# Performance work log

Hardware: AMD Instinct MI355X
Metric: run time of the kernel (lower is better)

The kernel has to match this reference:

```python
import jax, jax.numpy as jnp
import numpy as np

B, S, D = 64, 8192, 128  # batch, source length, hidden (enc == dec)


def setup_inputs() -> dict:
    key = jax.random.key(0)
    ks = jax.random.split(key, 7)
    s = 1.0 / np.sqrt(D)
    return {
        "input": jax.random.normal(ks[0], (B, D), jnp.float32),
        "context": jax.random.normal(ks[1], (B, S, D), jnp.float32),
        "W_enc": jax.random.uniform(ks[2], (D, D), jnp.float32, -s, s),
        "b_enc": jax.random.uniform(ks[3], (D,), jnp.float32, -s, s),
        "W_dec": jax.random.uniform(ks[4], (D, D), jnp.float32, -s, s),
        "b_dec": jax.random.uniform(ks[5], (D,), jnp.float32, -s, s),
        "W_out": jax.random.uniform(ks[6], (D, 2 * D), jnp.float32, -s, s),  # no bias
    }


def reference(input, context, W_enc, b_enc, W_dec, b_dec, W_out):
    # projected_context = tanh(lin_encoder(context))  [B, S, D]
    pc = jnp.tanh(jnp.einsum("bse,de->bsd", context, W_enc) + b_enc)
    # q = tanh(lin_decoder(input))  [B, D]
    q = jnp.tanh(input @ W_dec.T + b_dec)
    # attention scores via bmm(projected_context, q): [B, S]
    scores = jnp.einsum("bsd,bd->bs", pc, q)
    attn = jax.nn.softmax(scores, axis=1)  # softmax over source positions
    # weighted sum of (raw) context: [B, D]
    weighted_context = jnp.einsum("bs,bsd->bd", attn, context)
    # h_tilde = tanh(linear_out(concat(weighted_context, q)))  [B, D]
    h_tilde = jnp.tanh(jnp.concatenate([weighted_context, q], axis=-1) @ W_out.T)
    return h_tilde, attn
```

## Files before the change

### kernel.cpp

```cpp
#include <hip/hip_runtime.h>
#include <hip/hip_bf16.h>

#define BB 64
#define SS 8192
#define DD 128
#define NCHUNK 8
#define CHROWS 1024
#define NTILE 16

typedef __attribute__((ext_vector_type(8))) short bf16x8;
typedef __attribute__((ext_vector_type(4))) float f32x4;

#define SWZ(c, qd) ((qd) * 16 + ((c) ^ (2 * (qd))))

__device__ __forceinline__ unsigned pk2(float x, float y) {
    __hip_bfloat162 h = __float22bfloat162_rn(make_float2(x, y));
    union { __hip_bfloat162 h2; unsigned u; } cv;
    cv.h2 = h;
    return cv.u;
}

__device__ __forceinline__ float bflo(unsigned p) { return __uint_as_float(p << 16); }
__device__ __forceinline__ float bfhi(unsigned p) { return __uint_as_float(p & 0xffff0000u); }

__device__ __forceinline__ float tanh_fast(float x) {
    float e = __expf(2.f * x);
    return 1.f - 2.f / (e + 1.f);
}

__global__ void qproj_kernel(const float* __restrict__ input,
                             const float* __restrict__ W_dec,
                             const float* __restrict__ b_dec,
                             float* __restrict__ q) {
    __shared__ float xin[DD];
    const int b = blockIdx.x, d = threadIdx.x;
    xin[d] = input[b * DD + d];
    __syncthreads();
    const float4* wrow = (const float4*)(W_dec + (size_t)d * DD);
    float acc = 0.f;
#pragma unroll
    for (int k4 = 0; k4 < DD / 4; k4++) {
        float4 w = wrow[k4];
        float4 x = ((const float4*)xin)[k4];
        acc += w.x * x.x + w.y * x.y + w.z * x.z + w.w * x.w;
    }
    q[b * DD + d] = tanh_fast(acc + b_dec[d]);
}

__global__ __launch_bounds__(256, 2) void score_fused_kernel(
    const float* __restrict__ ctx,
    const float* __restrict__ W_enc,
    const float* __restrict__ b_enc,
    const float* __restrict__ q,
    float* __restrict__ scores,
    float* __restrict__ wcp,
    float* __restrict__ Mp,
    float* __restrict__ Tp) {
    __shared__ __align__(16) short Wl[16384];
    __shared__ __align__(16) short Cl[2][8192];
    __shared__ float sw[64];
    __shared__ float4 red[256];

    const int t = threadIdx.x;

    const float4* W4 = (const float4*)W_enc;
    for (int c2 = t; c2 < 2048; c2 += 256) {
        int row = c2 >> 4, kc = c2 & 15;
        float4 f0 = W4[row * 32 + kc * 2];
        float4 f1 = W4[row * 32 + kc * 2 + 1];
        int nt = row >> 4, colw = row & 15, kk = kc >> 2, qd = kc & 3;
        int a8 = (nt * 4 + kk) * 128 + SWZ(colw, qd) * 2;
        uint4 u;
        u.x = pk2(f0.x, f0.y); u.y = pk2(f0.z, f0.w);
        u.z = pk2(f1.x, f1.y); u.w = pk2(f1.z, f1.w);
        *(uint4*)&Wl[a8 * 4] = u;
    }

    const int wv = t >> 6, lane = t & 63;
    const int col = lane & 15, quad = lane >> 4;
    const int b = blockIdx.x >> 3;
    const int chunk = blockIdx.x & 7;

    const int u = t & 31, rg = t >> 5;
    const int ukk = u >> 3, uqd = (u >> 1) & 3, uh = u & 1;

    float qv[8], bv[8];
#pragma unroll
    for (int nt = 0; nt < 8; nt++) {
        qv[nt] = q[b * DD + nt * 16 + col];
        bv[nt] = b_enc[nt * 16 + col];
    }

    const float4* base = (const float4*)(ctx + ((size_t)b * SS + (size_t)chunk * CHROWS) * DD);

    float4 R[8];
    auto pack_tile = [&](int buf) {
#pragma unroll
        for (int i = 0; i < 8; i++) {
            int row = rg + 8 * i, w = row >> 4, c = row & 15;
            int a8 = (w * 4 + ukk) * 128 + SWZ(c, uqd) * 2 + uh;
            uint2 pk;
            pk.x = pk2(R[i].x, R[i].y);
            pk.y = pk2(R[i].z, R[i].w);
            *(uint2*)&Cl[buf][a8 * 4] = pk;
        }
    };

#pragma unroll
    for (int i = 0; i < 8; i++) R[i] = base[t + 256 * i];
    pack_tile(0);
    __syncthreads();

    float Mrun = -INFINITY, Trun = 0.f;
    float4 acc4 = {0.f, 0.f, 0.f, 0.f};

    for (int it = 0; it < NTILE; ++it) {
        const int cur = it & 1;
        if (it < NTILE - 1) {
            const float4* tb = base + (size_t)(it + 1) * 2048;
#pragma unroll
            for (int i = 0; i < 8; i++) R[i] = tb[t + 256 * i];
        }

        bf16x8 a[4];
#pragma unroll
        for (int kk = 0; kk < 4; kk++) {
            int a8 = (wv * 4 + kk) * 128 + SWZ(col, quad) * 2;
            a[kk] = *(const bf16x8*)&Cl[cur][a8 * 4];
        }
        f32x4 acc[8];
#pragma unroll
        for (int nt = 0; nt < 8; nt++) {
            f32x4 c = {0.f, 0.f, 0.f, 0.f};
#pragma unroll
            for (int kk = 0; kk < 4; kk++) {
                int a8 = (nt * 4 + kk) * 128 + SWZ(col, quad) * 2;
                bf16x8 bf = *(const bf16x8*)&Wl[a8 * 4];
                c = __builtin_amdgcn_mfma_f32_16x16x32_bf16(a[kk], bf, c, 0, 0, 0);
            }
            acc[nt] = c;
        }

#pragma unroll
        for (int r = 0; r < 4; r++) {
            float v = 0.f;
#pragma unroll
            for (int nt = 0; nt < 8; nt++)
                v += tanh_fast(acc[nt][r] + bv[nt]) * qv[nt];
            v += __shfl_xor(v, 1);
            v += __shfl_xor(v, 2);
            v += __shfl_xor(v, 4);
            v += __shfl_xor(v, 8);
            if (col == 0) {
                int lrow = wv * 16 + quad * 4 + r;
                sw[lrow] = v;
                scores[(size_t)b * SS + (size_t)chunk * CHROWS + it * 64 + lrow] = v;
            }
        }
        __syncthreads();

        float sv = sw[lane];
        float m = sv;
#pragma unroll
        for (int off = 1; off < 64; off <<= 1) m = fmaxf(m, __shfl_xor(m, off));
        float Mnew = fmaxf(Mrun, m);
        float alpha = __expf(Mrun - Mnew);
        float wlane = __expf(sv - Mnew);
        float ts = wlane;
#pragma unroll
        for (int off = 1; off < 64; off <<= 1) ts += __shfl_xor(ts, off);
        Trun = Trun * alpha + ts;
        Mrun = Mnew;

        acc4.x *= alpha; acc4.y *= alpha; acc4.z *= alpha; acc4.w *= alpha;
#pragma unroll
        for (int i = 0; i < 8; i++) {
            int row = rg + 8 * i, w = row >> 4, c = row & 15;
            int a8 = (w * 4 + ukk) * 128 + SWZ(c, uqd) * 2 + uh;
            uint2 pk = *(const uint2*)&Cl[cur][a8 * 4];
            float wi = __shfl(wlane, row);
            acc4.x += wi * bflo(pk.x);
            acc4.y += wi * bfhi(pk.x);
            acc4.z += wi * bflo(pk.y);
            acc4.w += wi * bfhi(pk.y);
        }

        if (it < NTILE - 1) pack_tile(cur ^ 1);

        __syncthreads();
    }

    red[t] = acc4;
    __syncthreads();
    if (t < 32) {
        float4 s = red[t];
#pragma unroll
        for (int k = 1; k < 8; k++) {
            float4 p = red[t + 32 * k];
            s.x += p.x; s.y += p.y; s.z += p.z; s.w += p.w;
        }
        *(float4*)&wcp[(size_t)blockIdx.x * DD + 4 * t] = s;
    }
    if (t == 0) {
        Mp[blockIdx.x] = Mrun;
        Tp[blockIdx.x] = Trun;
    }
}

__global__ void combine_out_kernel(const float* __restrict__ wcp,
                                   const float* __restrict__ Mp,
                                   const float* __restrict__ Tp,
                                   const float* __restrict__ q,
                                   const float* __restrict__ W_out,
                                   float* __restrict__ h,
                                   float* __restrict__ Ms,
                                   float* __restrict__ Tinv) {
    __shared__ float cat[2 * DD];
    const int b = blockIdx.x, d = threadIdx.x;
    float M = -INFINITY;
#pragma unroll
    for (int j = 0; j < NCHUNK; j++) M = fmaxf(M, Mp[b * NCHUNK + j]);
    float T = 0.f, acc = 0.f;
#pragma unroll
    for (int j = 0; j < NCHUNK; j++) {
        float e = __expf(Mp[b * NCHUNK + j] - M);
        T += Tp[b * NCHUNK + j] * e;
        acc += wcp[(size_t)(b * NCHUNK + j) * DD + d] * e;
    }
    float ti = 1.f / T;
    cat[d] = acc * ti;
    cat[DD + d] = q[b * DD + d];
    if (d == 0) { Ms[b] = M; Tinv[b] = ti; }
    __syncthreads();
    const float4* wrow = (const float4*)(W_out + (size_t)d * 2 * DD);
    float a2 = 0.f;
#pragma unroll
    for (int k4 = 0; k4 < 2 * DD / 4; k4++) {
        float4 w = wrow[k4];
        float4 x = ((const float4*)cat)[k4];
        a2 += w.x * x.x + w.y * x.y + w.z * x.z + w.w * x.w;
    }
    h[b * DD + d] = tanh_fast(a2);
}

__global__ __launch_bounds__(512) void attnfin_kernel(const float* __restrict__ scores,
                                                      const float* __restrict__ Ms,
                                                      const float* __restrict__ Tinv,
                                                      float* __restrict__ attn) {
    const int b = blockIdx.x >> 2, seg = blockIdx.x & 3;
    const float M = Ms[b], ti = Tinv[b];
    const float4* s4 = (const float4*)(scores + (size_t)b * SS) + seg * 512;
    float4* a4 = (float4*)(attn + (size_t)b * SS) + seg * 512;
    float4 v = s4[threadIdx.x];
    v.x = __expf(v.x - M) * ti;
    v.y = __expf(v.y - M) * ti;
    v.z = __expf(v.z - M) * ti;
    v.w = __expf(v.w - M) * ti;
    a4[threadIdx.x] = v;
}

extern "C" void kernel_launch(void* const* d_in, const int* in_sizes, int n_in,
                              void* d_out, int out_size, void* d_ws, size_t ws_size,
                              hipStream_t stream) {
    const float* input = (const float*)d_in[0];
    const float* ctx   = (const float*)d_in[1];
    const float* W_enc = (const float*)d_in[2];
    const float* b_enc = (const float*)d_in[3];
    const float* W_dec = (const float*)d_in[4];
    const float* b_dec = (const float*)d_in[5];
    const float* W_out = (const float*)d_in[6];

    float* h    = (float*)d_out;
    float* attn = (float*)d_out + BB * DD;

    float* ws     = (float*)d_ws;
    float* q      = ws;
    float* scores = ws + 8192;
    float* wcp    = scores + 524288;
    float* Mp     = wcp + 512 * DD;
    float* Tp     = Mp + 512;
    float* Ms     = Tp + 512;
    float* Tinv   = Ms + 64;

    qproj_kernel<<<BB, DD, 0, stream>>>(input, W_dec, b_dec, q);
    score_fused_kernel<<<BB * NCHUNK, 256, 0, stream>>>(ctx, W_enc, b_enc, q,
                                                        scores, wcp, Mp, Tp);
    combine_out_kernel<<<BB, DD, 0, stream>>>(wcp, Mp, Tp, q, W_out, h, Ms, Tinv);
    attnfin_kernel<<<BB * 4, 512, 0, stream>>>(scores, Ms, Tinv, attn);
}
```

Baseline: 400.3 us.

## Make each wave own its rows and drop per-tile block barriers

Each wavefront now loads, packs, scores and accumulates its own 16 rows of every 64-row tile, keeping a per-wave online-softmax state. Per-tile __syncthreads are removed and the LDS context buffer goes from double to single. The four per-wave partial states are merged with exp rescaling at the end. This removes block-wide barriers and halves context LDS, aiming for better latency hiding and occupancy. The cost is smaller per-wave global loads, and reuse of LDS and sw within a wave relies on implicit wave-synchronous ordering.

```diff
diff --git a/kernel.cpp b/kernel.cpp
--- a/kernel.cpp
+++ b/kernel.cpp
@@ -57,9 +57,10 @@
     float* __restrict__ Mp,
     float* __restrict__ Tp) {
     __shared__ __align__(16) short Wl[16384];
-    __shared__ __align__(16) short Cl[2][8192];
+    __shared__ __align__(16) short Cl[8192];
     __shared__ float sw[64];
-    __shared__ float4 red[256];
+    __shared__ float Mw[4], Tw[4];
+    __shared__ float4 red[128];
 
     const int t = threadIdx.x;
 
@@ -81,7 +82,7 @@
     const int b = blockIdx.x >> 3;
     const int chunk = blockIdx.x & 7;
 
-    const int u = t & 31, rg = t >> 5;
+    const int u = lane & 31, rg = lane >> 5;
     const int ukk = u >> 3, uqd = (u >> 1) & 3, uh = u & 1;
 
     float qv[8], bv[8];
@@ -91,42 +92,40 @@
         bv[nt] = b_enc[nt * 16 + col];
     }
 
-    const float4* base = (const float4*)(ctx + ((size_t)b * SS + (size_t)chunk * CHROWS) * DD);
+    const float4* base = (const float4*)(ctx
+        + ((size_t)b * SS + (size_t)chunk * CHROWS + wv * 16) * DD);
 
     float4 R[8];
-    auto pack_tile = [&](int buf) {
+#pragma unroll
+    for (int i = 0; i < 8; i++) R[i] = base[(2 * i + rg) * 32 + u];
+
+    __syncthreads();
+
+    float Mrun = -INFINITY, Trun = 0.f;
+    float4 acc4 = {0.f, 0.f, 0.f, 0.f};
+
+    for (int it = 0; it < NTILE; ++it) {
 #pragma unroll
         for (int i = 0; i < 8; i++) {
-            int row = rg + 8 * i, w = row >> 4, c = row & 15;
-            int a8 = (w * 4 + ukk) * 128 + SWZ(c, uqd) * 2 + uh;
+            int c = 2 * i + rg;
+            int a8 = (wv * 4 + ukk) * 128 + SWZ(c, uqd) * 2 + uh;
             uint2 pk;
             pk.x = pk2(R[i].x, R[i].y);
             pk.y = pk2(R[i].z, R[i].w);
-            *(uint2*)&Cl[buf][a8 * 4] = pk;
-        }
-    };
-
-#pragma unroll
-    for (int i = 0; i < 8; i++) R[i] = base[t + 256 * i];
-    pack_tile(0);
-    __syncthreads();
-
-    float Mrun = -INFINITY, Trun = 0.f;
-    float4 acc4 = {0.f, 0.f, 0.f, 0.f};
-
-    for (int it = 0; it < NTILE; ++it) {
-        const int cur = it & 1;
+            *(uint2*)&Cl[a8 * 4] = pk;
+        }
+
         if (it < NTILE - 1) {
-            const float4* tb = base + (size_t)(it + 1) * 2048;
-#pragma unroll
-            for (int i = 0; i < 8; i++) R[i] = tb[t + 256 * i];
+            const float4* nb = base + (size_t)(it + 1) * 2048;
+#pragma unroll
+            for (int i = 0; i < 8; i++) R[i] = nb[(2 * i + rg) * 32 + u];
         }
 
         bf16x8 a[4];
 #pragma unroll
         for (int kk = 0; kk < 4; kk++) {
             int a8 = (wv * 4 + kk) * 128 + SWZ(col, quad) * 2;
-            a[kk] = *(const bf16x8*)&Cl[cur][a8 * 4];
+            a[kk] = *(const bf16x8*)&Cl[a8 * 4];
         }
         f32x4 acc[8];
 #pragma unroll
@@ -141,6 +140,7 @@
             acc[nt] = c;
         }
 
+        float vr[4];
 #pragma unroll
         for (int r = 0; r < 4; r++) {
             float v = 0.f;
@@ -151,59 +151,69 @@
             v += __shfl_xor(v, 2);
             v += __shfl_xor(v, 4);
             v += __shfl_xor(v, 8);
-            if (col == 0) {
-                int lrow = wv * 16 + quad * 4 + r;
-                sw[lrow] = v;
-                scores[(size_t)b * SS + (size_t)chunk * CHROWS + it * 64 + lrow] = v;
-            }
-        }
-        __syncthreads();
-
-        float sv = sw[lane];
+            vr[r] = v;
+        }
+        if (col == 0) {
+#pragma unroll
+            for (int r = 0; r < 4; r++) sw[wv * 16 + quad * 4 + r] = vr[r];
+        }
+        float sv = sw[wv * 16 + (lane & 15)];
+
         float m = sv;
-#pragma unroll
-        for (int off = 1; off < 64; off <<= 1) m = fmaxf(m, __shfl_xor(m, off));
+        m = fmaxf(m, __shfl_xor(m, 1));
+        m = fmaxf(m, __shfl_xor(m, 2));
+        m = fmaxf(m, __shfl_xor(m, 4));
+        m = fmaxf(m, __shfl_xor(m, 8));
         float Mnew = fmaxf(Mrun, m);
         float alpha = __expf(Mrun - Mnew);
-        float wlane = __expf(sv - Mnew);
-        float ts = wlane;
-#pragma unroll
-        for (int off = 1; off < 64; off <<= 1) ts += __shfl_xor(ts, off);
+        float wl = __expf(sv - Mnew);
+        float ts = wl;
+        ts += __shfl_xor(ts, 1);
+        ts += __shfl_xor(ts, 2);
+        ts += __shfl_xor(ts, 4);
+        ts += __shfl_xor(ts, 8);
         Trun = Trun * alpha + ts;
         Mrun = Mnew;
 
+        if (lane < 16)
+            scores[(size_t)b * SS + (size_t)chunk * CHROWS + it * 64 + wv * 16 + lane] = sv;
+
         acc4.x *= alpha; acc4.y *= alpha; acc4.z *= alpha; acc4.w *= alpha;
 #pragma unroll
         for (int i = 0; i < 8; i++) {
-            int row = rg + 8 * i, w = row >> 4, c = row & 15;
-            int a8 = (w * 4 + ukk) * 128 + SWZ(c, uqd) * 2 + uh;
-            uint2 pk = *(const uint2*)&Cl[cur][a8 * 4];
-            float wi = __shfl(wlane, row);
+            int c = 2 * i + rg;
+            int a8 = (wv * 4 + ukk) * 128 + SWZ(c, uqd) * 2 + uh;
+            uint2 pk = *(const uint2*)&Cl[a8 * 4];
+            float wi = __shfl(wl, c);
             acc4.x += wi * bflo(pk.x);
             acc4.y += wi * bfhi(pk.x);
             acc4.z += wi * bflo(pk.y);
             acc4.w += wi * bfhi(pk.y);
         }
-
-        if (it < NTILE - 1) pack_tile(cur ^ 1);
-
-        __syncthreads();
-    }
-
-    red[t] = acc4;
+    }
+
+    acc4.x += __shfl_xor(acc4.x, 32);
+    acc4.y += __shfl_xor(acc4.y, 32);
+    acc4.z += __shfl_xor(acc4.z, 32);
+    acc4.w += __shfl_xor(acc4.w, 32);
+    if (lane < 32) red[wv * 32 + lane] = acc4;
+    if (lane == 0) { Mw[wv] = Mrun; Tw[wv] = Trun; }
     __syncthreads();
     if (t < 32) {
-        float4 s = red[t];
-#pragma unroll
-        for (int k = 1; k < 8; k++) {
-            float4 p = red[t + 32 * k];
-            s.x += p.x; s.y += p.y; s.z += p.z; s.w += p.w;
-        }
+        float M = fmaxf(fmaxf(Mw[0], Mw[1]), fmaxf(Mw[2], Mw[3]));
+        float e0 = __expf(Mw[0] - M), e1 = __expf(Mw[1] - M);
+        float e2 = __expf(Mw[2] - M), e3 = __expf(Mw[3] - M);
+        float4 p0 = red[t], p1 = red[32 + t], p2 = red[64 + t], p3 = red[96 + t];
+        float4 s;
+        s.x = p0.x * e0 + p1.x * e1 + p2.x * e2 + p3.x * e3;
+        s.y = p0.y * e0 + p1.y * e1 + p2.y * e2 + p3.y * e3;
+        s.z = p0.z * e0 + p1.z * e1 + p2.z * e2 + p3.z * e3;
+        s.w = p0.w * e0 + p1.w * e1 + p2.w * e2 + p3.w * e3;
         *(float4*)&wcp[(size_t)blockIdx.x * DD + 4 * t] = s;
-    }
-    if (t == 0) {
-        Mp[blockIdx.x] = Mrun;
-        Tp[blockIdx.x] = Trun;
+        if (t == 0) {
+            Mp[blockIdx.x] = M;
+            Tp[blockIdx.x] = Tw[0] * e0 + Tw[1] * e1 + Tw[2] * e2 + Tw[3] * e3;
+        }
     }
 }
 
```

Result: slower. 415.5 us (+3.8%).

## Double-buffer context prefetch in registers and reuse packed tile for weighted sum

Applied to the files above, without the earlier changes.

The tile loop is unrolled by two, with two register buffers for global context loads, so each load is issued about two tiles ahead of its use instead of one. Each thread also keeps its packed bf16 values in registers and reuses them for the softmax-weighted sum, instead of reading them back from shared memory. The aim is to hide more global-load latency and remove some LDS traffic. The extra 48 or so VGPRs per thread, under launch_bounds(256,2), risk spilling or lower occupancy.

```diff
diff --git a/kernel.cpp b/kernel.cpp
--- a/kernel.cpp
+++ b/kernel.cpp
@@ -46,6 +46,25 @@
     }
     q[b * DD + d] = tanh_fast(acc + b_dec[d]);
 }
+
+#define ISSUE(tile, R) do {                                          \
+    const float4* tb_ = base + (size_t)(tile) * 2048;                \
+    _Pragma("unroll")                                                \
+    for (int i = 0; i < 8; i++) R[i] = tb_[t + 256 * i];             \
+} while (0)
+
+#define PACK(buf, R) do {                                            \
+    _Pragma("unroll")                                                \
+    for (int i = 0; i < 8; i++) {                                    \
+        int row_ = rg + 8 * i, w_ = row_ >> 4, c_ = row_ & 15;       \
+        int a8_ = (w_ * 4 + ukk) * 128 + SWZ(c_, uqd) * 2 + uh;      \
+        uint2 pk_;                                                   \
+        pk_.x = pk2(R[i].x, R[i].y);                                 \
+        pk_.y = pk2(R[i].z, R[i].w);                                 \
+        P[i] = pk_;                                                  \
+        *(uint2*)&Cl[buf][a8_ * 4] = pk_;                            \
+    }                                                                \
+} while (0)
 
 __global__ __launch_bounds__(256, 2) void score_fused_kernel(
     const float* __restrict__ ctx,
@@ -93,35 +112,13 @@
 
     const float4* base = (const float4*)(ctx + ((size_t)b * SS + (size_t)chunk * CHROWS) * DD);
 
-    float4 R[8];
-    auto pack_tile = [&](int buf) {
-#pragma unroll
-        for (int i = 0; i < 8; i++) {
-            int row = rg + 8 * i, w = row >> 4, c = row & 15;
-            int a8 = (w * 4 + ukk) * 128 + SWZ(c, uqd) * 2 + uh;
-            uint2 pk;
-            pk.x = pk2(R[i].x, R[i].y);
-            pk.y = pk2(R[i].z, R[i].w);
-            *(uint2*)&Cl[buf][a8 * 4] = pk;
-        }
-    };
-
-#pragma unroll
-    for (int i = 0; i < 8; i++) R[i] = base[t + 256 * i];
-    pack_tile(0);
-    __syncthreads();
+    float4 RA[8], RB[8];
+    uint2 P[8];
 
     float Mrun = -INFINITY, Trun = 0.f;
     float4 acc4 = {0.f, 0.f, 0.f, 0.f};
 
-    for (int it = 0; it < NTILE; ++it) {
-        const int cur = it & 1;
-        if (it < NTILE - 1) {
-            const float4* tb = base + (size_t)(it + 1) * 2048;
-#pragma unroll
-            for (int i = 0; i < 8; i++) R[i] = tb[t + 256 * i];
-        }
-
+    auto compute_tile = [&](int it, int cur) {
         bf16x8 a[4];
 #pragma unroll
         for (int kk = 0; kk < 4; kk++) {
@@ -140,7 +137,6 @@
             }
             acc[nt] = c;
         }
-
 #pragma unroll
         for (int r = 0; r < 4; r++) {
             float v = 0.f;
@@ -157,8 +153,9 @@
                 scores[(size_t)b * SS + (size_t)chunk * CHROWS + it * 64 + lrow] = v;
             }
         }
-        __syncthreads();
-
+    };
+
+    auto softmax_wsum = [&]() {
         float sv = sw[lane];
         float m = sv;
 #pragma unroll
@@ -175,19 +172,40 @@
         acc4.x *= alpha; acc4.y *= alpha; acc4.z *= alpha; acc4.w *= alpha;
 #pragma unroll
         for (int i = 0; i < 8; i++) {
-            int row = rg + 8 * i, w = row >> 4, c = row & 15;
-            int a8 = (w * 4 + ukk) * 128 + SWZ(c, uqd) * 2 + uh;
-            uint2 pk = *(const uint2*)&Cl[cur][a8 * 4];
+            int row = rg + 8 * i;
+            uint2 pk = P[i];
             float wi = __shfl(wlane, row);
             acc4.x += wi * bflo(pk.x);
             acc4.y += wi * bfhi(pk.x);
             acc4.z += wi * bflo(pk.y);
             acc4.w += wi * bfhi(pk.y);
         }
-
-        if (it < NTILE - 1) pack_tile(cur ^ 1);
-
+    };
+
+    ISSUE(0, RA);
+    ISSUE(1, RB);
+    PACK(0, RA);
+    __syncthreads();
+
+    for (int it2 = 0; it2 < NTILE / 2; ++it2) {
+        const int T = 2 * it2;
+        const bool more = (it2 < NTILE / 2 - 1);
+
+        compute_tile(T, 0);
         __syncthreads();
+        softmax_wsum();
+        if (more) ISSUE(T + 2, RA);
+        PACK(1, RB);
+        __syncthreads();
+
+        compute_tile(T + 1, 1);
+        __syncthreads();
+        softmax_wsum();
+        if (more) {
+            ISSUE(T + 3, RB);
+            PACK(0, RA);
+            __syncthreads();
+        }
     }
 
     red[t] = acc4;
```

After: 426.6 us. 6.6% more time.
